# Kernel tuning notes

Measured on AMD Instinct MI355X. Metric: run time of the kernel, lower is better.

Reference implementation:

```python
import jax, jax.numpy as jnp
import numpy as np

N_NODES = 50000


def rgcn_conv(x, src, dst, edge_type, W, root, bias):
    """PyG RGCNConv: out[i] = x[i] @ root + bias + sum_r mean_{j in N_r(i)} x[j] @ W[r].
    W: [R, F_in, F_out]. Mean aggregation is per-relation (PyG default aggr='mean')."""
    num_rel = W.shape[0]
    n = x.shape[0]
    out = x @ root + bias
    x_src = x[src]  # [E, F_in] gather once
    for r in range(num_rel):  # small fixed relation count
        mask = (edge_type == r)
        msg = jnp.where(mask[:, None], x_src, 0.0) @ W[r]          # [E, F_out]
        s = jax.ops.segment_sum(msg, dst, num_segments=n)           # [N, F_out]
        c = jax.ops.segment_sum(mask.astype(x.dtype), dst, num_segments=n)  # [N]
        out = out + s / jnp.maximum(c, 1.0)[:, None]
    return out


def setup_inputs() -> dict:
    key = jax.random.key(0)
    ks = jax.random.split(key, 10)
    N, E, F_in, F_hid, F_out, R = N_NODES, 800000, 128, 128, 64, 8
    x = jax.random.normal(ks[0], (N, F_in), dtype=jnp.float32)
    edge_index = jax.random.randint(ks[1], (2, E), 0, N, dtype=jnp.int64)
    edge_type = jax.random.randint(ks[2], (E,), 0, R, dtype=jnp.int64)
    s1 = 1.0 / np.sqrt(F_in)
    s2 = 1.0 / np.sqrt(F_hid)
    W1 = jax.random.normal(ks[3], (R, F_in, F_hid), dtype=jnp.float32) * s1
    root1 = jax.random.normal(ks[4], (F_in, F_hid), dtype=jnp.float32) * s1
    b1 = jnp.zeros((F_hid,), dtype=jnp.float32)
    W2 = jax.random.normal(ks[5], (R, F_hid, F_out), dtype=jnp.float32) * s2
    root2 = jax.random.normal(ks[6], (F_hid, F_out), dtype=jnp.float32) * s2
    b2 = jnp.zeros((F_out,), dtype=jnp.float32)
    return {"x": x, "edge_index": edge_index, "edge_type": edge_type,
            "W1": W1, "root1": root1, "b1": b1,
            "W2": W2, "root2": root2, "b2": b2}


def reference(x, edge_index, edge_type, W1, root1, b1, W2, root2, b2):
    src, dst = edge_index[0], edge_index[1]
    h = jax.nn.relu(rgcn_conv(x, src, dst, edge_type, W1, root1, b1))
    out = rgcn_conv(h, src, dst, edge_type, W2, root2, b2)
    return out
```

## Files before the change

### kernel.cpp

```cpp
#include <hip/hip_runtime.h>

#define N_NODES 50000
#define N_EDGES 800000
#define R_REL   8

#define TNBKT   3125
#define TCAP    512
#define SLAB    2048
#define BINBLK  ((N_EDGES + SLAB - 1) / SLAB)

typedef float  f32x4  __attribute__((ext_vector_type(4)));
typedef __bf16 bf16x8 __attribute__((ext_vector_type(8)));

__device__ __forceinline__ unsigned short f2bf(float f) {
    unsigned int u = __float_as_uint(f);
    u = (u + 0x7FFFu + ((u >> 16) & 1u)) >> 16;
    return (unsigned short)u;
}
__device__ __forceinline__ float bflo(unsigned int u) { return __uint_as_float(u << 16); }
__device__ __forceinline__ float bfhi(unsigned int u) { return __uint_as_float(u & 0xFFFF0000u); }

__device__ __forceinline__ void acc16(float* a, uint4 u0, uint4 u1) {
    a[0]  += bflo(u0.x);   a[1]  += bfhi(u0.x);
    a[2]  += bflo(u0.y);   a[3]  += bfhi(u0.y);
    a[4]  += bflo(u0.z);   a[5]  += bfhi(u0.z);
    a[6]  += bflo(u0.w);   a[7]  += bfhi(u0.w);
    a[8]  += bflo(u1.x);   a[9]  += bfhi(u1.x);
    a[10] += bflo(u1.y);   a[11] += bfhi(u1.y);
    a[12] += bflo(u1.z);   a[13] += bfhi(u1.z);
    a[14] += bflo(u1.w);   a[15] += bfhi(u1.w);
}


__global__ __launch_bounds__(256) void k_bin(
    const int* __restrict__ src, const int* __restrict__ dst,
    const int* __restrict__ et, int* __restrict__ gcur,
    unsigned* __restrict__ gbin)
{
    __shared__ int hist[TNBKT];
    __shared__ int base[TNBKT];
    const int t = threadIdx.x;
    const int e0 = blockIdx.x * SLAB;
    for (int i = t; i < TNBKT; i += 256) hist[i] = 0;
    __syncthreads();
#pragma unroll
    for (int i = 0; i < SLAB / 256; ++i) {
        int e = e0 + i * 256 + t;
        if (e < N_EDGES) atomicAdd(&hist[dst[e] >> 4], 1);
    }
    __syncthreads();
    for (int i = t; i < TNBKT; i += 256) {
        int h = hist[i];
        base[i] = (h > 0) ? atomicAdd(&gcur[i], h) : 0;
        hist[i] = 0;
    }
    __syncthreads();
#pragma unroll
    for (int i = 0; i < SLAB / 256; ++i) {
        int e = e0 + i * 256 + t;
        if (e < N_EDGES) {
            int d = dst[e];
            int b = d >> 4;
            int sub = atomicAdd(&hist[b], 1);
            int pos = base[b] + sub;
            unsigned rec = ((unsigned)src[e] << 7) | (unsigned)((d & 15) * 8 + et[e]);
            if (pos < TCAP) gbin[(size_t)b * TCAP + pos] = rec;
        }
    }
}


#define W1_ELEMS (9 * 128 * 128)
#define W2_ELEMS (9 * 64 * 128)
#define N4       (N_NODES * 32)

__global__ __launch_bounds__(256) void k_cvtw(
    const float* __restrict__ x, unsigned short* __restrict__ xb,
    const float* __restrict__ root1, const float* __restrict__ W1,
    const float* __restrict__ root2, const float* __restrict__ W2,
    unsigned short* __restrict__ Wt1, unsigned short* __restrict__ Wt2,
    int* __restrict__ gcur)
{
    const int idx = blockIdx.x * 256 + threadIdx.x;
    if (idx < TNBKT) gcur[idx] = 0;
    if (idx < N4) {
        float4 v = *(const float4*)(x + (size_t)idx * 4);
        ushort4 o;
        o.x = f2bf(v.x); o.y = f2bf(v.y); o.z = f2bf(v.z); o.w = f2bf(v.w);
        *(ushort4*)(xb + (size_t)idx * 4) = o;
    }
    if (idx < W1_ELEMS) {
        int j    = idx & 7;
        int lane = (idx >> 3) & 63;
        int r    = idx >> 9;
        int nb   = r & 7;
        int r2   = r >> 3;
        int kk   = r2 & 3;
        int seg  = r2 >> 2;
        int k = kk * 32 + (lane >> 4) * 8 + j;
        int n = nb * 16 + (lane & 15);
        float v = (seg == 0) ? root1[k * 128 + n] : W1[((seg - 1) * 128 + k) * 128 + n];
        Wt1[idx] = f2bf(v);
    } else if (idx < W1_ELEMS + W2_ELEMS) {
        int i2   = idx - W1_ELEMS;
        int j    = i2 & 7;
        int lane = (i2 >> 3) & 63;
        int r    = i2 >> 9;
        int nb   = r & 3;
        int r2   = r >> 2;
        int kk   = r2 & 3;
        int seg  = r2 >> 2;
        int k = kk * 32 + (lane >> 4) * 8 + j;
        int n = nb * 16 + (lane & 15);
        float v = (seg == 0) ? root2[k * 64 + n] : W2[((seg - 1) * 128 + k) * 64 + n];
        Wt2[i2] = f2bf(v);
    }
}


template <int FOUT, bool RELU, bool OUT_BF16>
__global__ __launch_bounds__(512) void k_fused(
    const unsigned short* __restrict__ xin,
    const unsigned short* __restrict__ WtP,
    const float* __restrict__ bias,
    const int* __restrict__ gcnt,
    const unsigned* __restrict__ gbin,
    unsigned short* __restrict__ outb,
    float* __restrict__ outf)
{
    constexpr int NBt = FOUT / 16;
    __shared__ __align__(16) unsigned short As0[16][136];
    __shared__ __align__(16) unsigned short As[8][16][136];
    __shared__ unsigned short sorted[TCAP];
    __shared__ int dcnt[128];
    __shared__ int kbeg[128];
    __shared__ int kcur[128];

    const int t = threadIdx.x;
    const int node0 = blockIdx.x * 16;

    if (t < 128) { dcnt[t] = 0; kcur[t] = 0; }
    if (t < 128) {
        const int sr = t >> 3;
        const int sp = t & 7;
        const uint4* s4 = (const uint4*)(xin + (size_t)(node0 + sr) * 128 + sp * 16);
        uint4 r0 = s4[0], r1 = s4[1];
        uint4* d = (uint4*)&As0[sr][sp * 16];
        d[0] = r0; d[1] = r1;
    }
    const int nraw = gcnt[blockIdx.x];
    const int n = nraw < TCAP ? nraw : TCAP;
    unsigned rec = 0;
    if (t < n) rec = gbin[(size_t)blockIdx.x * TCAP + t];
    __syncthreads();

    if (t < n) atomicAdd(&dcnt[rec & 127], 1);
    __syncthreads();

    if (t < 64) {
        int d0 = dcnt[2 * t], d1 = dcnt[2 * t + 1];
        int s = d0 + d1;
        int inc = s;
#pragma unroll
        for (int off = 1; off < 64; off <<= 1) {
            int y = __shfl_up(inc, off, 64);
            if (t >= off) inc += y;
        }
        int excl = inc - s;
        kbeg[2 * t]     = excl;
        kbeg[2 * t + 1] = excl + d0;
    }
    __syncthreads();

    if (t < n) {
        int key = rec & 127;
        int pos = atomicAdd(&kcur[key], 1);
        sorted[kbeg[key] + pos] = (unsigned short)(rec >> 7);
    }
    __syncthreads();

    {
        const int key = t >> 2;
        const int q   = t & 3;
        const int rel = key & 7;
        const int nl  = key >> 3;

        const int beg = kbeg[key];
        const int deg = dcnt[key];
        const int end = beg + deg;

        const unsigned short* bx = xin + q * 32;
        float a[32];
#pragma unroll
        for (int i = 0; i < 32; ++i) a[i] = 0.f;

        int j = beg;
        for (; j + 1 < end; j += 2) {
            int s0 = sorted[j];
            int s1 = sorted[j + 1];
            const uint4* p0 = (const uint4*)(bx + (size_t)s0 * 128);
            const uint4* p1 = (const uint4*)(bx + (size_t)s1 * 128);
            uint4 v0 = p0[0], v1 = p0[1], v2 = p0[2], v3 = p0[3];
            uint4 w0 = p1[0], w1 = p1[1], w2 = p1[2], w3 = p1[3];
            acc16(a, v0, v1);
            acc16(a + 16, v2, v3);
            acc16(a, w0, w1);
            acc16(a + 16, w2, w3);
        }
        if (j < end) {
            int s = sorted[j];
            const uint4* p = (const uint4*)(bx + (size_t)s * 128);
            uint4 v0 = p[0], v1 = p[1], v2 = p[2], v3 = p[3];
            acc16(a, v0, v1);
            acc16(a + 16, v2, v3);
        }

        float scl = 1.f / (float)(deg > 1 ? deg : 1);
        unsigned int pk[16];
#pragma unroll
        for (int i = 0; i < 16; ++i)
            pk[i] = (unsigned int)f2bf(a[i * 2] * scl) |
                    ((unsigned int)f2bf(a[i * 2 + 1] * scl) << 16);
        uint4* G = (uint4*)&As[rel][nl][0];
        const int g0 = q * 4;
        G[(g0 + 0) ^ rel] = make_uint4(pk[0],  pk[1],  pk[2],  pk[3]);
        G[(g0 + 1) ^ rel] = make_uint4(pk[4],  pk[5],  pk[6],  pk[7]);
        G[(g0 + 2) ^ rel] = make_uint4(pk[8],  pk[9],  pk[10], pk[11]);
        G[(g0 + 3) ^ rel] = make_uint4(pk[12], pk[13], pk[14], pk[15]);
    }

    __syncthreads();

    const int lane = t & 63;
    const int w = t >> 6;
    if (w >= NBt) return;
    const int quad = lane >> 4;
    const int tc = lane & 15;

    f32x4 acc = (f32x4){0.f, 0.f, 0.f, 0.f};
    const bf16x8* Bp = (const bf16x8*)WtP;

#pragma unroll
    for (int seg = 0; seg < 9; ++seg) {
        const uint4* Ag = (seg == 0) ? (const uint4*)&As0[tc][0]
                                     : (const uint4*)&As[seg - 1][tc][0];
        const int s = (seg == 0) ? 0 : (seg - 1);
#pragma unroll
        for (int kk = 0; kk < 4; ++kk) {
            bf16x8 af = *(const bf16x8*)(Ag + (((kk << 2) + quad) ^ s));
            bf16x8 bf = Bp[((seg * 4 + kk) * NBt + w) * 64 + lane];
            acc = __builtin_amdgcn_mfma_f32_16x16x32_bf16(af, bf, acc, 0, 0, 0);
        }
    }

    const int col = w * 16 + tc;
    const float bs = bias[col];
#pragma unroll
    for (int i = 0; i < 4; ++i) {
        int r = node0 + quad * 4 + i;
        float v = acc[i] + bs;
        if (RELU) v = fmaxf(v, 0.f);
        if (OUT_BF16) outb[(size_t)r * FOUT + col] = f2bf(v);
        else          outf[(size_t)r * FOUT + col] = v;
    }
}


extern "C" void kernel_launch(void* const* d_in, const int* in_sizes, int n_in,
                              void* d_out, int out_size, void* d_ws, size_t ws_size,
                              hipStream_t stream) {
    const float* x     = (const float*)d_in[0];
    const int*   ei    = (const int*)d_in[1];
    const int*   et    = (const int*)d_in[2];
    const float* W1    = (const float*)d_in[3];
    const float* root1 = (const float*)d_in[4];
    const float* b1    = (const float*)d_in[5];
    const float* W2    = (const float*)d_in[6];
    const float* root2 = (const float*)d_in[7];
    const float* b2    = (const float*)d_in[8];
    float* out = (float*)d_out;

    int* ws = (int*)d_ws;
    int* gcur = ws;
    unsigned* gbin = (unsigned*)(gcur + 3200);
    unsigned short* xb  = (unsigned short*)(gbin + (size_t)TNBKT * TCAP);
    unsigned short* hb  = xb + (size_t)N_NODES * 128;
    unsigned short* Wt1 = hb + (size_t)N_NODES * 128;
    unsigned short* Wt2 = Wt1 + W1_ELEMS;

    const int* esrc = ei;
    const int* edst = ei + N_EDGES;

    k_cvtw<<<(N4 + 255) / 256, 256, 0, stream>>>(x, xb, root1, W1, root2, W2,
                                                 Wt1, Wt2, gcur);
    k_bin<<<BINBLK, 256, 0, stream>>>(esrc, edst, et, gcur, gbin);

    const int NT = N_NODES / 16;

    k_fused<128, true,  true ><<<NT, 512, 0, stream>>>(xb, Wt1, b1, gcur, gbin, hb, nullptr);
    k_fused<64,  false, false><<<NT, 512, 0, stream>>>(hb, Wt2, b2, gcur, gbin, nullptr, out);
}
```

Measured before the change: 254.6 us.

## Merge binning and conversion kernels; software-pipeline neighbor gathers in aggregation

Combines the edge-binning kernel and the bf16 conversion kernel into one launch whose leading blocks bin edges and whose trailing blocks convert x and the weights. The counter reset moves to a memset so the two jobs can run concurrently. The aggregation loop now prefetches the next pair of neighbor rows before accumulating the current pair, hiding gather latency. To make this safe, the sorted array is padded and zeroed so prefetches past the end read row 0. The cost is extra registers and some wasted loads per key.

```diff
diff --git a/kernel.cpp b/kernel.cpp
--- a/kernel.cpp
+++ b/kernel.cpp
@@ -32,57 +32,57 @@
 }
 
 
-__global__ __launch_bounds__(256) void k_bin(
+#define W1_ELEMS (9 * 128 * 128)
+#define W2_ELEMS (9 * 64 * 128)
+#define N4       (N_NODES * 32)
+#define NB_CVT   ((N4 + 255) / 256)
+#define NB_PREP  (BINBLK + NB_CVT)
+
+__global__ __launch_bounds__(256) void k_prep(
     const int* __restrict__ src, const int* __restrict__ dst,
     const int* __restrict__ et, int* __restrict__ gcur,
-    unsigned* __restrict__ gbin)
+    unsigned* __restrict__ gbin,
+    const float* __restrict__ x, unsigned short* __restrict__ xb,
+    const float* __restrict__ root1, const float* __restrict__ W1,
+    const float* __restrict__ root2, const float* __restrict__ W2,
+    unsigned short* __restrict__ Wt1, unsigned short* __restrict__ Wt2)
 {
     __shared__ int hist[TNBKT];
     __shared__ int base[TNBKT];
     const int t = threadIdx.x;
-    const int e0 = blockIdx.x * SLAB;
-    for (int i = t; i < TNBKT; i += 256) hist[i] = 0;
-    __syncthreads();
-#pragma unroll
-    for (int i = 0; i < SLAB / 256; ++i) {
-        int e = e0 + i * 256 + t;
-        if (e < N_EDGES) atomicAdd(&hist[dst[e] >> 4], 1);
-    }
-    __syncthreads();
-    for (int i = t; i < TNBKT; i += 256) {
-        int h = hist[i];
-        base[i] = (h > 0) ? atomicAdd(&gcur[i], h) : 0;
-        hist[i] = 0;
-    }
-    __syncthreads();
-#pragma unroll
-    for (int i = 0; i < SLAB / 256; ++i) {
-        int e = e0 + i * 256 + t;
-        if (e < N_EDGES) {
-            int d = dst[e];
-            int b = d >> 4;
-            int sub = atomicAdd(&hist[b], 1);
-            int pos = base[b] + sub;
-            unsigned rec = ((unsigned)src[e] << 7) | (unsigned)((d & 15) * 8 + et[e]);
-            if (pos < TCAP) gbin[(size_t)b * TCAP + pos] = rec;
-        }
-    }
-}
-
-
-#define W1_ELEMS (9 * 128 * 128)
-#define W2_ELEMS (9 * 64 * 128)
-#define N4       (N_NODES * 32)
-
-__global__ __launch_bounds__(256) void k_cvtw(
-    const float* __restrict__ x, unsigned short* __restrict__ xb,
-    const float* __restrict__ root1, const float* __restrict__ W1,
-    const float* __restrict__ root2, const float* __restrict__ W2,
-    unsigned short* __restrict__ Wt1, unsigned short* __restrict__ Wt2,
-    int* __restrict__ gcur)
-{
-    const int idx = blockIdx.x * 256 + threadIdx.x;
-    if (idx < TNBKT) gcur[idx] = 0;
+
+    if (blockIdx.x < BINBLK) {
+        const int e0 = blockIdx.x * SLAB;
+        for (int i = t; i < TNBKT; i += 256) hist[i] = 0;
+        __syncthreads();
+#pragma unroll
+        for (int i = 0; i < SLAB / 256; ++i) {
+            int e = e0 + i * 256 + t;
+            if (e < N_EDGES) atomicAdd(&hist[dst[e] >> 4], 1);
+        }
+        __syncthreads();
+        for (int i = t; i < TNBKT; i += 256) {
+            int h = hist[i];
+            base[i] = (h > 0) ? atomicAdd(&gcur[i], h) : 0;
+            hist[i] = 0;
+        }
+        __syncthreads();
+#pragma unroll
+        for (int i = 0; i < SLAB / 256; ++i) {
+            int e = e0 + i * 256 + t;
+            if (e < N_EDGES) {
+                int d = dst[e];
+                int b = d >> 4;
+                int sub = atomicAdd(&hist[b], 1);
+                int pos = base[b] + sub;
+                unsigned rec = ((unsigned)src[e] << 7) | (unsigned)((d & 15) * 8 + et[e]);
+                if (pos < TCAP) gbin[(size_t)b * TCAP + pos] = rec;
+            }
+        }
+        return;
+    }
+
+    const int idx = (blockIdx.x - BINBLK) * 256 + t;
     if (idx < N4) {
         float4 v = *(const float4*)(x + (size_t)idx * 4);
         ushort4 o;
@@ -131,7 +131,7 @@
     constexpr int NBt = FOUT / 16;
     __shared__ __align__(16) unsigned short As0[16][136];
     __shared__ __align__(16) unsigned short As[8][16][136];
-    __shared__ unsigned short sorted[TCAP];
+    __shared__ unsigned short sorted[TCAP + 8];
     __shared__ int dcnt[128];
     __shared__ int kbeg[128];
     __shared__ int kcur[128];
@@ -140,6 +140,8 @@
     const int node0 = blockIdx.x * 16;
 
     if (t < 128) { dcnt[t] = 0; kcur[t] = 0; }
+    sorted[t] = 0;
+    if (t < 8) sorted[TCAP + t] = 0;
     if (t < 128) {
         const int sr = t >> 3;
         const int sp = t & 7;
@@ -195,24 +197,32 @@
         for (int i = 0; i < 32; ++i) a[i] = 0.f;
 
         int j = beg;
+        int sA = sorted[j];
+        int sB = sorted[j + 1];
+        const uint4* pA = (const uint4*)(bx + (size_t)sA * 128);
+        const uint4* pB = (const uint4*)(bx + (size_t)sB * 128);
+        uint4 A0 = pA[0], A1 = pA[1], A2 = pA[2], A3 = pA[3];
+        uint4 B0 = pB[0], B1 = pB[1], B2 = pB[2], B3 = pB[3];
+
         for (; j + 1 < end; j += 2) {
-            int s0 = sorted[j];
-            int s1 = sorted[j + 1];
-            const uint4* p0 = (const uint4*)(bx + (size_t)s0 * 128);
-            const uint4* p1 = (const uint4*)(bx + (size_t)s1 * 128);
-            uint4 v0 = p0[0], v1 = p0[1], v2 = p0[2], v3 = p0[3];
-            uint4 w0 = p1[0], w1 = p1[1], w2 = p1[2], w3 = p1[3];
-            acc16(a, v0, v1);
-            acc16(a + 16, v2, v3);
-            acc16(a, w0, w1);
-            acc16(a + 16, w2, w3);
+            int sC = sorted[j + 2];
+            int sD = sorted[j + 3];
+            const uint4* pC = (const uint4*)(bx + (size_t)sC * 128);
+            const uint4* pD = (const uint4*)(bx + (size_t)sD * 128);
+            uint4 C0 = pC[0], C1 = pC[1], C2 = pC[2], C3 = pC[3];
+            uint4 D0 = pD[0], D1 = pD[1], D2 = pD[2], D3 = pD[3];
+
+            acc16(a, A0, A1);
+            acc16(a + 16, A2, A3);
+            acc16(a, B0, B1);
+            acc16(a + 16, B2, B3);
+
+            A0 = C0; A1 = C1; A2 = C2; A3 = C3;
+            B0 = D0; B1 = D1; B2 = D2; B3 = D3;
         }
         if (j < end) {
-            int s = sorted[j];
-            const uint4* p = (const uint4*)(bx + (size_t)s * 128);
-            uint4 v0 = p[0], v1 = p[1], v2 = p[2], v3 = p[3];
-            acc16(a, v0, v1);
-            acc16(a + 16, v2, v3);
+            acc16(a, A0, A1);
+            acc16(a + 16, A2, A3);
         }
 
         float scl = 1.f / (float)(deg > 1 ? deg : 1);
@@ -291,9 +301,9 @@
     const int* esrc = ei;
     const int* edst = ei + N_EDGES;
 
-    k_cvtw<<<(N4 + 255) / 256, 256, 0, stream>>>(x, xb, root1, W1, root2, W2,
-                                                 Wt1, Wt2, gcur);
-    k_bin<<<BINBLK, 256, 0, stream>>>(esrc, edst, et, gcur, gbin);
+    hipMemsetAsync(gcur, 0, 3200 * sizeof(int), stream);
+    k_prep<<<NB_PREP, 256, 0, stream>>>(esrc, edst, et, gcur, gbin,
+                                        x, xb, root1, W1, root2, W2, Wt1, Wt2);
 
     const int NT = N_NODES / 16;
 
```

Result: no change. 251.8 us (-1.1%).

## Merge edge binning and conversion into one kernel using direct global atomics

Applied to the files above, without the earlier changes.

Replaces the two-pass shared-memory histogram binning kernel with one global atomicAdd per edge. That scatter is folded into the same launch as the x/weight bf16 conversion, with separate block ranges for each job. The bucket counters are now cleared with hipMemsetAsync, which removes the kernel-to-kernel dependency and the shared-memory histogram passes. The cost is heavier contention on global atomics (800k atomics over 3125 counters) and an extra memset call.

```diff
diff --git a/kernel.cpp b/kernel.cpp
--- a/kernel.cpp
+++ b/kernel.cpp
@@ -6,8 +6,6 @@
 
 #define TNBKT   3125
 #define TCAP    512
-#define SLAB    2048
-#define BINBLK  ((N_EDGES + SLAB - 1) / SLAB)
 
 typedef float  f32x4  __attribute__((ext_vector_type(4)));
 typedef __bf16 bf16x8 __attribute__((ext_vector_type(8)));
@@ -32,57 +30,39 @@
 }
 
 
-__global__ __launch_bounds__(256) void k_bin(
-    const int* __restrict__ src, const int* __restrict__ dst,
-    const int* __restrict__ et, int* __restrict__ gcur,
-    unsigned* __restrict__ gbin)
-{
-    __shared__ int hist[TNBKT];
-    __shared__ int base[TNBKT];
-    const int t = threadIdx.x;
-    const int e0 = blockIdx.x * SLAB;
-    for (int i = t; i < TNBKT; i += 256) hist[i] = 0;
-    __syncthreads();
-#pragma unroll
-    for (int i = 0; i < SLAB / 256; ++i) {
-        int e = e0 + i * 256 + t;
-        if (e < N_EDGES) atomicAdd(&hist[dst[e] >> 4], 1);
-    }
-    __syncthreads();
-    for (int i = t; i < TNBKT; i += 256) {
-        int h = hist[i];
-        base[i] = (h > 0) ? atomicAdd(&gcur[i], h) : 0;
-        hist[i] = 0;
-    }
-    __syncthreads();
-#pragma unroll
-    for (int i = 0; i < SLAB / 256; ++i) {
-        int e = e0 + i * 256 + t;
-        if (e < N_EDGES) {
-            int d = dst[e];
-            int b = d >> 4;
-            int sub = atomicAdd(&hist[b], 1);
-            int pos = base[b] + sub;
-            unsigned rec = ((unsigned)src[e] << 7) | (unsigned)((d & 15) * 8 + et[e]);
-            if (pos < TCAP) gbin[(size_t)b * TCAP + pos] = rec;
-        }
-    }
-}
-
-
 #define W1_ELEMS (9 * 128 * 128)
 #define W2_ELEMS (9 * 64 * 128)
 #define N4       (N_NODES * 32)
-
-__global__ __launch_bounds__(256) void k_cvtw(
+#define NB_SCAT  (N_EDGES / 256)
+#define NB_CVT   ((N4 + 255) / 256)
+#define NB_PREP  (NB_SCAT + NB_CVT)
+
+__global__ __launch_bounds__(256) void k_prep(
+    const int* __restrict__ src, const int* __restrict__ dst,
+    const int* __restrict__ et, int* __restrict__ gcur,
+    unsigned* __restrict__ gbin,
     const float* __restrict__ x, unsigned short* __restrict__ xb,
     const float* __restrict__ root1, const float* __restrict__ W1,
     const float* __restrict__ root2, const float* __restrict__ W2,
-    unsigned short* __restrict__ Wt1, unsigned short* __restrict__ Wt2,
-    int* __restrict__ gcur)
+    unsigned short* __restrict__ Wt1, unsigned short* __restrict__ Wt2)
 {
-    const int idx = blockIdx.x * 256 + threadIdx.x;
-    if (idx < TNBKT) gcur[idx] = 0;
+    const int t = threadIdx.x;
+
+    if (blockIdx.x < NB_SCAT) {
+        const int e = blockIdx.x * 256 + t;
+        int d  = dst[e];
+        int s  = src[e];
+        int r  = et[e];
+        int b  = d >> 4;
+        int pos = atomicAdd(&gcur[b], 1);
+        if (pos < TCAP) {
+            unsigned rec = ((unsigned)s << 7) | (unsigned)((d & 15) * 8 + r);
+            gbin[(size_t)b * TCAP + pos] = rec;
+        }
+        return;
+    }
+
+    const int idx = (blockIdx.x - NB_SCAT) * 256 + t;
     if (idx < N4) {
         float4 v = *(const float4*)(x + (size_t)idx * 4);
         ushort4 o;
@@ -291,9 +271,9 @@
     const int* esrc = ei;
     const int* edst = ei + N_EDGES;
 
-    k_cvtw<<<(N4 + 255) / 256, 256, 0, stream>>>(x, xb, root1, W1, root2, W2,
-                                                 Wt1, Wt2, gcur);
-    k_bin<<<BINBLK, 256, 0, stream>>>(esrc, edst, et, gcur, gbin);
+    hipMemsetAsync(gcur, 0, 3200 * sizeof(int), stream);
+    k_prep<<<NB_PREP, 256, 0, stream>>>(esrc, edst, et, gcur, gbin,
+                                        x, xb, root1, W1, root2, W2, Wt1, Wt2);
 
     const int NT = N_NODES / 16;
 
```

Result: slower. 291.7 us (+14.5%).
